# Performance work log

Measured on AMD Instinct MI355X. Metric: run time of the kernel, lower is better.

## Reference

```python
import jax, jax.numpy as jnp
import numpy as np

B = 32; NPG = 500; N = B * NPG; E = 256000; F = 1024; OD = 128
DD = 80; TD = 32; NH = 4; DH = TD // NH; DFF = 128; NL = 2
LSUB = 128; MAXLEN = 4 * LSUB
NEG = -1e9; SLOPE = 0.01; EPS = 1e-5


def setup_inputs() -> dict:
    key = jax.random.key(0)
    ks = iter(jax.random.split(key, 64))
    nrm = lambda *s: jax.random.normal(next(ks), s, jnp.float32)
    w = lambda *s: nrm(*s) * 0.02
    inp = {}
    inp["pro1_x"] = nrm(N, F)
    inp["pro2_x"] = nrm(N, F)
    inp["pro1_edge_index"] = jax.random.randint(next(ks), (2, E), 0, N)
    inp["pro2_edge_index"] = jax.random.randint(next(ks), (2, E), 0, N)
    inp["pro1_batch"] = jnp.repeat(jnp.arange(B), NPG)
    inp["pro2_batch"] = jnp.repeat(jnp.arange(B), NPG)
    for nm in ("mas1_straight", "mas1_flipped", "mas2_straight", "mas2_flipped"):
        inp[nm] = nrm(B, LSUB, DD)
        inp[nm + "_lengths"] = jax.random.randint(next(ks), (B,), 1, LSUB + 1)
    inp["gcn1_w"] = w(F, F); inp["gcn1_b"] = jnp.zeros(F)
    inp["gcn2_w"] = w(F, F); inp["gcn2_b"] = jnp.zeros(F)
    inp["fc1_w"] = w(OD, F); inp["fc1_b"] = jnp.zeros(OD)
    inp["fc2_w"] = w(OD, F); inp["fc2_b"] = jnp.zeros(OD)
    inp["red_w"] = w(TD - 2, DD); inp["red_b"] = jnp.zeros(TD - 2)
    inp["attn_in_w"] = w(NL, 3 * TD, TD); inp["attn_in_b"] = jnp.zeros((NL, 3 * TD))
    inp["attn_out_w"] = w(NL, TD, TD); inp["attn_out_b"] = jnp.zeros((NL, TD))
    inp["ln1_w"] = jnp.ones((NL, TD)); inp["ln1_b"] = jnp.zeros((NL, TD))
    inp["ln2_w"] = jnp.ones((NL, TD)); inp["ln2_b"] = jnp.zeros((NL, TD))
    inp["ff1_w"] = w(NL, DFF, TD); inp["ff1_b"] = jnp.zeros((NL, DFF))
    inp["ff2_w"] = w(NL, TD, DFF); inp["ff2_b"] = jnp.zeros((NL, TD))
    inp["final_w"] = w(1, 2 * OD + TD); inp["final_b"] = jnp.zeros(1)
    return inp


def _leaky(v):
    return jnp.where(v >= 0, v, SLOPE * v)


def _gcn(x, ei, W, b):
    # GCNConv: x' = D^-1/2 (A + I) D^-1/2 (x @ W^T) + b
    sl = jnp.arange(N, dtype=ei.dtype)
    src = jnp.concatenate([ei[0], sl])
    dst = jnp.concatenate([ei[1], sl])
    deg = jax.ops.segment_sum(jnp.ones(src.shape[0], x.dtype), dst, N)
    dinv = jax.lax.rsqrt(deg)
    norm = (dinv[src] * dinv[dst])[:, None]
    h = x @ W.T
    return jax.ops.segment_sum(h[src] * norm, dst, N) + b


def _gmp(x, batch):
    # global mean pool per graph
    s = jax.ops.segment_sum(x, batch, B)
    c = jax.ops.segment_sum(jnp.ones(x.shape[0], x.dtype), batch, B)
    return s / c[:, None]


def _ln(x, w, b):
    m = x.mean(-1, keepdims=True)
    v = ((x - m) ** 2).mean(-1, keepdims=True)
    return (x - m) * jax.lax.rsqrt(v + EPS) * w + b


def _forward(pro1_x, pro1_edge_index, pro1_batch, pro2_x, pro2_edge_index, pro2_batch,
             mas1_straight, mas1_flipped, mas2_straight, mas2_flipped,
             mas1_straight_lengths, mas1_flipped_lengths, mas2_straight_lengths, mas2_flipped_lengths,
             gcn1_w, gcn1_b, fc1_w, fc1_b, gcn2_w, gcn2_b, fc2_w, fc2_b,
             red_w, red_b, attn_in_w, attn_in_b, attn_out_w, attn_out_b,
             ln1_w, ln1_b, ln2_w, ln2_b, ff1_w, ff1_b, ff2_w, ff2_b,
             final_w, final_b):
    # --- graph branches (dropout = identity at inference) ---
    x1 = _leaky(_gcn(pro1_x, pro1_edge_index, gcn1_w, gcn1_b))
    x1 = _leaky(_gmp(x1, pro1_batch) @ fc1_w.T + fc1_b)           # [B, OD]
    x2 = _leaky(_gcn(pro2_x, pro2_edge_index, gcn2_w, gcn2_b))
    x2 = _leaky(_gmp(x2, pro2_batch) @ fc2_w.T + fc2_b)           # [B, OD]

    # --- vectorized ragged pack: project, append indicators, scatter to offsets ---
    inds = ((1.0, 1.0), (0.0, 1.0), (1.0, 0.0), (0.0, 0.0))      # (straight, first)
    mas = (mas1_straight, mas1_flipped, mas2_straight, mas2_flipped)
    lens = (mas1_straight_lengths, mas1_flipped_lengths, mas2_straight_lengths, mas2_flipped_lengths)
    pos = jnp.arange(LSUB)
    brow = jnp.arange(B)[:, None]
    seq = jnp.zeros((B, MAXLEN, TD), jnp.float32)
    off = jnp.zeros((B,), lens[0].dtype)
    for m, l, (si, fi) in zip(mas, lens, inds):
        proj = m @ red_w.T + red_b                                # [B, LSUB, TD-2]
        ones = jnp.ones((B, LSUB, 1), jnp.float32)
        p = jnp.concatenate([proj, si * ones, fi * ones], -1)    # [B, LSUB, TD]
        valid = pos[None, :] < l[:, None]                        # [B, LSUB]
        idx = jnp.where(valid, off[:, None] + pos[None, :], 0)
        seq = seq.at[brow, idx].add(p * valid[..., None])
        off = off + l
    mask = jnp.arange(MAXLEN)[None, :] < off[:, None]            # [B, MAXLEN] True = valid

    # --- post-norm TransformerEncoder (relu FFN, key padding mask) ---
    x_t = seq
    for li in range(NL):
        qkv = x_t @ attn_in_w[li].T + attn_in_b[li]
        q, k, v = jnp.split(qkv, 3, axis=-1)
        q = q.reshape(B, MAXLEN, NH, DH)
        k = k.reshape(B, MAXLEN, NH, DH)
        v = v.reshape(B, MAXLEN, NH, DH)
        scores = jnp.einsum('bqhd,bkhd->bhqk', q, k) / np.float32(np.sqrt(DH))
        scores = jnp.where(mask[:, None, None, :], scores, NEG)
        attn = jax.nn.softmax(scores, axis=-1)
        o = jnp.einsum('bhqk,bkhd->bqhd', attn, v).reshape(B, MAXLEN, TD)
        o = o @ attn_out_w[li].T + attn_out_b[li]
        x_t = _ln(x_t + o, ln1_w[li], ln1_b[li])
        h = jax.nn.relu(x_t @ ff1_w[li].T + ff1_b[li]) @ ff2_w[li].T + ff2_b[li]
        x_t = _ln(x_t + h, ln2_w[li], ln2_b[li])

    mf = mask[..., None].astype(jnp.float32)
    mas_out = (x_t * mf).sum(1) / mf.sum(1)                      # masked mean [B, TD]

    combined = jnp.concatenate([x1, x2, mas_out], axis=1)        # [B, 2*OD + TD]
    return combined @ final_w.T + final_b                        # [B, 1]


def reference(pro1_x, pro1_edge_index, pro1_batch, pro2_x, pro2_edge_index, pro2_batch,
              mas1_straight, mas1_flipped, mas2_straight, mas2_flipped,
              mas1_straight_lengths, mas1_flipped_lengths, mas2_straight_lengths, mas2_flipped_lengths,
              gcn1_w, gcn1_b, fc1_w, fc1_b, gcn2_w, gcn2_b, fc2_w, fc2_b,
              red_w, red_b, attn_in_w, attn_in_b, attn_out_w, attn_out_b,
              ln1_w, ln1_b, ln2_w, ln2_b, ff1_w, ff1_b, ff2_w, ff2_b,
              final_w, final_b):
    return _forward(pro1_x, pro1_edge_index, pro1_batch, pro2_x, pro2_edge_index, pro2_batch,
                    mas1_straight, mas1_flipped, mas2_straight, mas2_flipped,
                    mas1_straight_lengths, mas1_flipped_lengths, mas2_straight_lengths, mas2_flipped_lengths,
                    gcn1_w, gcn1_b, fc1_w, fc1_b, gcn2_w, gcn2_b, fc2_w, fc2_b,
                    red_w, red_b, attn_in_w, attn_in_b, attn_out_w, attn_out_b,
                    ln1_w, ln1_b, ln2_w, ln2_b, ff1_w, ff1_b, ff2_w, ff2_b,
                    final_w, final_b)
```

## Files before the change

kernel.cpp:

```cpp
#include <hip/hip_runtime.h>
#include <stdint.h>

#define N_NODES 16000
#define B_      32
#define NPG_    500
#define E_      256000
#define F_      1024
#define OD_     128
#define DD_     80
#define TD_     32
#define NH_     4
#define DH_     8
#define DFF_    128
#define LSUB_   128
#define MAXLEN_ 512
#define EPS_    1e-5f
#define SLOPE_  0.01f

typedef __bf16 bf16x8 __attribute__((ext_vector_type(8)));
typedef float  f32x4  __attribute__((ext_vector_type(4)));

__device__ __forceinline__ float leaky(float v) { return v >= 0.f ? v : SLOPE_ * v; }

__device__ __forceinline__ unsigned short f2bf(float f) {
  unsigned u = __float_as_uint(f);
  u += 0x7FFFu + ((u >> 16) & 1u);
  return (unsigned short)(u >> 16);
}
__device__ __forceinline__ float bf2f(unsigned short u) {
  return __uint_as_float((unsigned)u << 16);
}

__device__ __forceinline__ void gld_lds16(const void* g, void* l) {
  __builtin_amdgcn_global_load_lds(
      (const __attribute__((address_space(1))) unsigned int*)g,
      (__attribute__((address_space(3))) unsigned int*)l, 16, 0, 0);
}

__global__ void k_f2bf2(const float* __restrict__ in0, const float* __restrict__ in1,
                        unsigned short* __restrict__ out0, unsigned short* __restrict__ out1,
                        int n4) {
  const float* in = blockIdx.y ? in1 : in0;
  unsigned short* out = blockIdx.y ? out1 : out0;
  int i = blockIdx.x * blockDim.x + threadIdx.x;
  int stride = gridDim.x * blockDim.x;
  for (; i < n4; i += stride) {
    float4 v = ((const float4*)in)[i];
    ushort4 o;
    o.x = f2bf(v.x); o.y = f2bf(v.y); o.z = f2bf(v.z); o.w = f2bf(v.w);
    ((ushort4*)out)[i] = o;
  }
}

__global__ __launch_bounds__(256) void k_gemm_bf16(const unsigned short* __restrict__ A,
                                                   const unsigned short* __restrict__ Bw,
                                                   unsigned short* __restrict__ C) {
  const int K = 1024, N = 1024;
  const size_t g = blockIdx.z;
  A  += g * (size_t)N_NODES * K;
  Bw += g * (size_t)K * N;
  C  += g * (size_t)N_NODES * N;
  __shared__ short As[128 * 32];
  __shared__ short Bs[128 * 32];
  const int t    = threadIdx.x;
  const int lane = t & 63, wave = t >> 6;
  const int wrow = wave >> 1, wcol = wave & 1;
  const int quad = lane >> 4, l15 = lane & 15;
  const int mBase = blockIdx.x * 128;
  const int nBase = blockIdx.y * 128;

  f32x4 acc[4][4];
  f32x4 zero = {0.f, 0.f, 0.f, 0.f};
#pragma unroll
  for (int i = 0; i < 4; ++i)
#pragma unroll
    for (int j = 0; j < 4; ++j) acc[i][j] = zero;

  const int r4 = t >> 2;
  const int c4 = (((t & 3) - ((t >> 3) & 3)) & 3) * 8;
  const int rs = ((quad + (l15 >> 1)) & 3) * 8;

  for (int kt = 0; kt < 32; ++kt) {
    const int k0 = kt * 32;
    gld_lds16(&A[(size_t)(mBase + r4) * K + k0 + c4],       &As[t * 8]);
    gld_lds16(&A[(size_t)(mBase + 64 + r4) * K + k0 + c4],  &As[2048 + t * 8]);
    gld_lds16(&Bw[(size_t)(nBase + r4) * K + k0 + c4],      &Bs[t * 8]);
    gld_lds16(&Bw[(size_t)(nBase + 64 + r4) * K + k0 + c4], &Bs[2048 + t * 8]);
    __syncthreads();

    bf16x8 a[4], b[4];
#pragma unroll
    for (int ti = 0; ti < 4; ++ti)
      a[ti] = *(const bf16x8*)&As[(wrow * 64 + ti * 16 + l15) * 32 + rs];
#pragma unroll
    for (int tj = 0; tj < 4; ++tj)
      b[tj] = *(const bf16x8*)&Bs[(wcol * 64 + tj * 16 + l15) * 32 + rs];
#pragma unroll
    for (int ti = 0; ti < 4; ++ti)
#pragma unroll
      for (int tj = 0; tj < 4; ++tj)
        acc[ti][tj] = __builtin_amdgcn_mfma_f32_16x16x32_bf16(a[ti], b[tj], acc[ti][tj], 0, 0, 0);
    __syncthreads();
  }

#pragma unroll
  for (int ti = 0; ti < 4; ++ti)
#pragma unroll
    for (int tj = 0; tj < 4; ++tj)
#pragma unroll
      for (int r = 0; r < 4; ++r) {
        int grow = mBase + wrow * 64 + ti * 16 + quad * 4 + r;
        int gcol = nBase + wcol * 64 + tj * 16 + l15;
        C[(size_t)grow * N + gcol] = f2bf(acc[ti][tj][r]);
      }
}

__global__ void k_hist(const int* __restrict__ ei0, const int* __restrict__ ei1,
                       int* __restrict__ cnt, int e, int n) {
  const int g = blockIdx.y;
  const int* dst = (g ? ei1 : ei0) + e;
  int i = blockIdx.x * 256 + threadIdx.x;
  if (i < e) atomicAdd(&cnt[g * n + dst[i]], 1);
}

__global__ void k_scan(const int* __restrict__ cnt_all, int* __restrict__ rowstart_all,
                       int* __restrict__ cursor_all, float* __restrict__ dinv_all, int n) {
  const int g = blockIdx.x;
  const int* cnt = cnt_all + g * n;
  int* rowstart = rowstart_all + g * (n + 1);
  int* cursor   = cursor_all + g * n;
  float* dinv   = dinv_all + g * n;
  __shared__ int part[256];
  __shared__ int base[257];
  int t = threadIdx.x;
  int chunk = (n + 255) >> 8;
  int s = 0;
  for (int j = 0; j < chunk; ++j) {
    int idx = t * chunk + j;
    if (idx < n) s += cnt[idx];
  }
  part[t] = s;
  __syncthreads();
  if (t == 0) {
    int a = 0;
    for (int i = 0; i < 256; ++i) { base[i] = a; a += part[i]; }
    base[256] = a;
  }
  __syncthreads();
  int a = base[t];
  for (int j = 0; j < chunk; ++j) {
    int idx = t * chunk + j;
    if (idx < n) {
      int c = cnt[idx];
      rowstart[idx] = a; cursor[idx] = a; a += c;
      dinv[idx] = rsqrtf((float)c + 1.0f);
    }
  }
  if (t == 0) rowstart[n] = base[256];
}

__global__ void k_scatter(const int* __restrict__ ei0, const int* __restrict__ ei1,
                          const float* __restrict__ dinv_all, int* __restrict__ cursor_all,
                          int* __restrict__ csr_all, float* __restrict__ csrw_all,
                          int e, int n) {
  const int g = blockIdx.y;
  const int* ei = g ? ei1 : ei0;
  int i = blockIdx.x * 256 + threadIdx.x;
  if (i < e) {
    int s = ei[i], d = ei[e + i];
    int p = atomicAdd(&cursor_all[g * n + d], 1);
    csr_all[(size_t)g * e + p]  = s;
    csrw_all[(size_t)g * e + p] = dinv_all[g * n + s] * dinv_all[g * n + d];
  }
}

__global__ __launch_bounds__(64) void k_gather(const ushort2* __restrict__ h2,
                                               const float* __restrict__ dinv,
                                               const int* __restrict__ rowstart,
                                               const int* __restrict__ csr,
                                               const float* __restrict__ csrw,
                                               ushort2* __restrict__ agg2) {
  const int sl = blockIdx.x;
  const int i  = blockIdx.y;
  const int t  = threadIdx.x;
  __shared__ int   ssrc[64];
  __shared__ float sw[64];
  const float di = dinv[i];
  const size_t fo = (size_t)sl * 64 + t;
  ushort2 sv = h2[(size_t)i * 512 + fo];
  const float selfw = di * di;
  float ax = bf2f(sv.x) * selfw, ay = bf2f(sv.y) * selfw;
  const int beg = rowstart[i], end = rowstart[i + 1];
  for (int base = beg; base < end; base += 64) {
    int c = end - base; if (c > 64) c = 64;
    __syncthreads();
    if (t < c) { ssrc[t] = csr[base + t]; sw[t] = csrw[base + t]; }
    __syncthreads();
    int j = 0;
    for (; j + 4 <= c; j += 4) {
      ushort2 v0 = h2[(size_t)ssrc[j]     * 512 + fo];
      ushort2 v1 = h2[(size_t)ssrc[j + 1] * 512 + fo];
      ushort2 v2 = h2[(size_t)ssrc[j + 2] * 512 + fo];
      ushort2 v3 = h2[(size_t)ssrc[j + 3] * 512 + fo];
      float w0 = sw[j], w1 = sw[j + 1], w2 = sw[j + 2], w3 = sw[j + 3];
      ax += bf2f(v0.x) * w0 + bf2f(v1.x) * w1 + bf2f(v2.x) * w2 + bf2f(v3.x) * w3;
      ay += bf2f(v0.y) * w0 + bf2f(v1.y) * w1 + bf2f(v2.y) * w2 + bf2f(v3.y) * w3;
    }
    for (; j < c; ++j) {
      ushort2 v0 = h2[(size_t)ssrc[j] * 512 + fo];
      float w0 = sw[j];
      ax += bf2f(v0.x) * w0; ay += bf2f(v0.y) * w0;
    }
  }
  ushort2 o; o.x = f2bf(ax); o.y = f2bf(ay);
  agg2[(size_t)i * 512 + fo] = o;
}

__global__ void k_pool(const unsigned short* __restrict__ agg_all,
                       const float* __restrict__ bias0, const float* __restrict__ bias1,
                       float* __restrict__ pooled_all) {
  int f = blockIdx.x * 256 + threadIdx.x;
  int z = blockIdx.z;
  int g = z >> 5, b = z & 31;
  const unsigned short* agg = agg_all + (size_t)g * N_NODES * F_;
  const float* bias = g ? bias1 : bias0;
  float* pooled = pooled_all + (size_t)g * B_ * F_;
  int r0 = blockIdx.y * 100;
  float bf = bias[f];
  float s = 0.f;
  for (int r = 0; r < 100; ++r)
    s += leaky(bf2f(agg[(size_t)(b * NPG_ + r0 + r) * F_ + f]) + bf);
  atomicAdd(&pooled[b * F_ + f], s);
}

__global__ void k_fc(const float* __restrict__ pooled_all,
                     const float* __restrict__ w0, const float* __restrict__ w1,
                     const float* __restrict__ bias0, const float* __restrict__ bias1,
                     float* __restrict__ out0, float* __restrict__ out1) {
  int b = blockIdx.x, o = threadIdx.x, g = blockIdx.y;
  const float* p  = pooled_all + (size_t)g * B_ * F_ + b * F_;
  const float* wr = (g ? w1 : w0) + o * F_;
  const float* bias = g ? bias1 : bias0;
  float* out = g ? out1 : out0;
  float acc = 0.f;
  for (int f = 0; f < F_; ++f) acc += p[f] * wr[f];
  out[b * OD_ + o] = leaky(acc * (1.f / 500.f) + bias[o]);
}

__global__ void k_pack(const float* __restrict__ m0, const float* __restrict__ m1,
                       const float* __restrict__ m2, const float* __restrict__ m3,
                       const int* __restrict__ l0, const int* __restrict__ l1,
                       const int* __restrict__ l2, const int* __restrict__ l3,
                       const float* __restrict__ rw, const float* __restrict__ rb,
                       float* __restrict__ seq) {
  __shared__ float xs[DD_];
  const int p = blockIdx.x, b = blockIdx.y, k = blockIdx.z;
  const float* mas = (k == 0) ? m0 : (k == 1) ? m1 : (k == 2) ? m2 : m3;
  const int*   lk  = (k == 0) ? l0 : (k == 1) ? l1 : (k == 2) ? l2 : l3;
  const int len = lk[b];
  if (p >= len) return;
  int off = 0;
  if (k > 0) off += l0[b];
  if (k > 1) off += l1[b];
  if (k > 2) off += l2[b];
  const int t = threadIdx.x;
  for (int d = t; d < DD_; d += 64) xs[d] = mas[(size_t)(b * LSUB_ + p) * DD_ + d];
  __syncthreads();
  if (t < TD_) {
    float v;
    if (t < TD_ - 2) {
      float a = rb[t];
      const float* w = &rw[t * DD_];
      for (int d = 0; d < DD_; ++d) a += xs[d] * w[d];
      v = a;
    } else if (t == TD_ - 2) {
      v = (k == 0 || k == 2) ? 1.f : 0.f;
    } else {
      v = (k < 2) ? 1.f : 0.f;
    }
    seq[((size_t)b * MAXLEN_ + off + p) * TD_ + t] = v;
  }
}

__global__ void k_totlen(const int* __restrict__ l0, const int* __restrict__ l1,
                         const int* __restrict__ l2, const int* __restrict__ l3,
                         int* __restrict__ tot) {
  int b = threadIdx.x;
  if (b < B_) tot[b] = l0[b] + l1[b] + l2[b] + l3[b];
}

__global__ void k_qkv(const float* __restrict__ xt, const float* __restrict__ w,
                      const float* __restrict__ bias, const int* __restrict__ tot,
                      float* __restrict__ qkv) {
  __shared__ float xs[TD_];
  const int row = blockIdx.x;
  if ((row & (MAXLEN_ - 1)) >= tot[row >> 9]) return;
  const int t = threadIdx.x;
  if (t < TD_) xs[t] = xt[(size_t)row * TD_ + t];
  __syncthreads();
  if (t < 3 * TD_) {
    float a = bias[t];
    const float* wr = &w[t * TD_];
#pragma unroll
    for (int k = 0; k < TD_; ++k) a += xs[k] * wr[k];
    qkv[(size_t)row * 96 + t] = a;
  }
}

__global__ __launch_bounds__(128) void k_attn(const float* __restrict__ qkv,
                                              const int* __restrict__ tot,
                                              float* __restrict__ obuf) {
  __shared__ float Kl[MAXLEN_ * DH_];
  __shared__ float Vl[MAXLEN_ * DH_];
  const int h = blockIdx.x, b = blockIdx.y, qz = blockIdx.z;
  const int t = threadIdx.x;
  const int L = tot[b];
  if (qz * 64 >= L) return;
  const float* base = &qkv[(size_t)b * MAXLEN_ * 96];
  for (int i = t; i < L * DH_; i += 128) {
    int p = i >> 3, d = i & 7;
    Kl[i] = base[p * 96 + 32 + h * 8 + d];
    Vl[i] = base[p * 96 + 64 + h * 8 + d];
  }
  __syncthreads();
  const int qi = qz * 64 + (t >> 1);
  if (qi >= L) return;
  const int half = t & 1;
  const float scale = 0.35355339059327373f;
  float q[8];
#pragma unroll
  for (int d = 0; d < 8; ++d) q[d] = base[qi * 96 + h * 8 + d] * scale;

  float l0 = 0.f, l1 = 0.f;
  float a0[8] = {0, 0, 0, 0, 0, 0, 0, 0};
  float a1[8] = {0, 0, 0, 0, 0, 0, 0, 0};
  int j = half;
  for (; j + 2 < L; j += 4) {
    const float* kr0 = &Kl[j * 8];
    const float* kr1 = &Kl[(j + 2) * 8];
    float s0 = 0.f, s1 = 0.f;
#pragma unroll
    for (int d = 0; d < 8; ++d) { s0 += q[d] * kr0[d]; s1 += q[d] * kr1[d]; }
    float p0 = __expf(s0), p1 = __expf(s1);
    l0 += p0; l1 += p1;
    const float* vr0 = &Vl[j * 8];
    const float* vr1 = &Vl[(j + 2) * 8];
#pragma unroll
    for (int d = 0; d < 8; ++d) { a0[d] += p0 * vr0[d]; a1[d] += p1 * vr1[d]; }
  }
  for (; j < L; j += 2) {
    const float* kr = &Kl[j * 8];
    float s = 0.f;
#pragma unroll
    for (int d = 0; d < 8; ++d) s += q[d] * kr[d];
    float p = __expf(s);
    l0 += p;
    const float* vr = &Vl[j * 8];
#pragma unroll
    for (int d = 0; d < 8; ++d) a0[d] += p * vr[d];
  }
  float l = l0 + l1;
#pragma unroll
  for (int d = 0; d < 8; ++d) a0[d] += a1[d];
  l += __shfl_xor(l, 1);
#pragma unroll
  for (int d = 0; d < 8; ++d) a0[d] += __shfl_xor(a0[d], 1);
  float inv = 1.f / l;
  const int dbase = half * 4;
  float4 o;
  o.x = a0[dbase + 0] * inv; o.y = a0[dbase + 1] * inv;
  o.z = a0[dbase + 2] * inv; o.w = a0[dbase + 3] * inv;
  *(float4*)&obuf[((size_t)b * MAXLEN_ + qi) * TD_ + h * 8 + dbase] = o;
}

__global__ void k_oproj_ln(const float* __restrict__ obuf, const float* __restrict__ w,
                           const float* __restrict__ bias, const float* __restrict__ lw,
                           const float* __restrict__ lb, const int* __restrict__ tot,
                           float* __restrict__ xt) {
  const int t = threadIdx.x;
  const int r = blockIdx.x * 8 + (t >> 5);
  if ((r & (MAXLEN_ - 1)) >= tot[r >> 9]) return;
  const int j = t & 31;
  const float* orow = &obuf[(size_t)r * TD_];
  float a = bias[j] + xt[(size_t)r * TD_ + j];
  const float* wr = &w[j * TD_];
#pragma unroll
  for (int k = 0; k < TD_; ++k) a += orow[k] * wr[k];
  float s1 = a, s2 = a * a;
#pragma unroll
  for (int m = 1; m < 32; m <<= 1) {
    s1 += __shfl_xor(s1, m, 32);
    s2 += __shfl_xor(s2, m, 32);
  }
  float mean = s1 * (1.f / 32.f);
  float var  = s2 * (1.f / 32.f) - mean * mean;
  xt[(size_t)r * TD_ + j] = (a - mean) * rsqrtf(var + EPS_) * lw[j] + lb[j];
}

__global__ void k_ffn_ln(const float* __restrict__ w1, const float* __restrict__ b1,
                         const float* __restrict__ w2, const float* __restrict__ b2,
                         const float* __restrict__ lw, const float* __restrict__ lb,
                         const int* __restrict__ tot, float* __restrict__ xt) {
  const int r = blockIdx.x, t = threadIdx.x;
  if ((r & (MAXLEN_ - 1)) >= tot[r >> 9]) return;
  __shared__ float xs[TD_];
  __shared__ float hb[DFF_];
  if (t < TD_) xs[t] = xt[(size_t)r * TD_ + t];
  __syncthreads();
  {
    float a = b1[t];
    const float* wr = &w1[t * TD_];
#pragma unroll
    for (int k = 0; k < TD_; ++k) a += xs[k] * wr[k];
    hb[t] = fmaxf(a, 0.f);
  }
  __syncthreads();
  if (t < TD_) {
    float a = b2[t] + xs[t];
    const float* wr = &w2[t * DFF_];
#pragma unroll
    for (int k = 0; k < DFF_; ++k) a += hb[k] * wr[k];
    float s1 = a, s2 = a * a;
#pragma unroll
    for (int m = 1; m < 32; m <<= 1) {
      s1 += __shfl_xor(s1, m, 32);
      s2 += __shfl_xor(s2, m, 32);
    }
    float mean = s1 * (1.f / 32.f);
    float var  = s2 * (1.f / 32.f) - mean * mean;
    xt[(size_t)r * TD_ + t] = (a - mean) * rsqrtf(var + EPS_) * lw[t] + lb[t];
  }
}

__global__ void k_maskmean(const float* __restrict__ xt, const int* __restrict__ tot,
                           float* __restrict__ mout) {
  __shared__ float sbuf[8][32];
  const int b = blockIdx.x, t = threadIdx.x;
  const int j = t & 31, c = t >> 5;
  const int L = tot[b];
  float s = 0.f;
  for (int p = c; p < L; p += 8) s += xt[((size_t)b * MAXLEN_ + p) * TD_ + j];
  sbuf[c][j] = s;
  __syncthreads();
  if (t < 32) {
    float a = 0.f;
#pragma unroll
    for (int cc = 0; cc < 8; ++cc) a += sbuf[cc][t];
    mout[b * TD_ + t] = a / (float)L;
  }
}

__global__ void k_final(const float* __restrict__ x1, const float* __restrict__ x2,
                        const float* __restrict__ mo, const float* __restrict__ fw,
                        const float* __restrict__ fb, float* __restrict__ out) {
  const int b = blockIdx.x, t = threadIdx.x;
  float s = 0.f;
  for (int i = t; i < 2 * OD_ + TD_; i += 64) {
    float c = (i < OD_) ? x1[b * OD_ + i]
            : (i < 2 * OD_) ? x2[b * OD_ + (i - OD_)]
            : mo[b * TD_ + (i - 2 * OD_)];
    s += fw[i] * c;
  }
#pragma unroll
  for (int m = 1; m < 64; m <<= 1) s += __shfl_xor(s, m, 64);
  if (t == 0) out[b] = s + fb[0];
}

extern "C" void kernel_launch(void* const* d_in, const int* in_sizes, int n_in,
                              void* d_out, int out_size, void* d_ws, size_t ws_size,
                              hipStream_t stream) {
  (void)in_sizes; (void)n_in; (void)out_size; (void)ws_size;
  const float* pro_x[2]  = {(const float*)d_in[0], (const float*)d_in[1]};
  const int*   pro_ei[2] = {(const int*)d_in[2], (const int*)d_in[3]};
  const float* mas[4]    = {(const float*)d_in[6], (const float*)d_in[8],
                            (const float*)d_in[10], (const float*)d_in[12]};
  const int*   lens[4]   = {(const int*)d_in[7], (const int*)d_in[9],
                            (const int*)d_in[11], (const int*)d_in[13]};
  const float* gw[2]  = {(const float*)d_in[14], (const float*)d_in[16]};
  const float* gb[2]  = {(const float*)d_in[15], (const float*)d_in[17]};
  const float* fcw[2] = {(const float*)d_in[18], (const float*)d_in[20]};
  const float* fcb[2] = {(const float*)d_in[19], (const float*)d_in[21]};
  const float* red_w = (const float*)d_in[22];
  const float* red_b = (const float*)d_in[23];
  const float* attn_in_w  = (const float*)d_in[24];
  const float* attn_in_b  = (const float*)d_in[25];
  const float* attn_out_w = (const float*)d_in[26];
  const float* attn_out_b = (const float*)d_in[27];
  const float* ln1_w = (const float*)d_in[28];
  const float* ln1_b = (const float*)d_in[29];
  const float* ln2_w = (const float*)d_in[30];
  const float* ln2_b = (const float*)d_in[31];
  const float* ff1_w = (const float*)d_in[32];
  const float* ff1_b = (const float*)d_in[33];
  const float* ff2_w = (const float*)d_in[34];
  const float* ff2_b = (const float*)d_in[35];
  const float* final_w = (const float*)d_in[36];
  const float* final_b = (const float*)d_in[37];
  float* out = (float*)d_out;

  char* p = (char*)d_ws;
  auto carve = [&](size_t bytes) -> void* {
    void* r = (void*)p;
    p += (bytes + 255) & ~(size_t)255;
    return r;
  };
  unsigned short* xb  = (unsigned short*)carve((size_t)2 * N_NODES * F_ * 2);
  unsigned short* Wb  = (unsigned short*)carve((size_t)2 * F_ * F_ * 2);
  unsigned short* h   = (unsigned short*)carve((size_t)2 * N_NODES * F_ * 2);
  unsigned short* agg = (unsigned short*)carve((size_t)2 * N_NODES * F_ * 2);
  int*   cnt      = (int*)carve((size_t)2 * N_NODES * 4);
  float* dinv     = (float*)carve((size_t)2 * N_NODES * 4);
  int*   rowstart = (int*)carve((size_t)2 * (N_NODES + 1) * 4);
  int*   cursor   = (int*)carve((size_t)2 * N_NODES * 4);
  int*   csr      = (int*)carve((size_t)2 * E_ * 4);
  float* csrw     = (float*)carve((size_t)2 * E_ * 4);
  float* pooled   = (float*)carve((size_t)2 * B_ * F_ * 4);
  float* xg[2];
  xg[0] = (float*)carve((size_t)B_ * OD_ * 4);
  xg[1] = (float*)carve((size_t)B_ * OD_ * 4);
  float* seq    = (float*)carve((size_t)B_ * MAXLEN_ * TD_ * 4);
  float* qkv    = (float*)carve((size_t)B_ * MAXLEN_ * 96 * 4);
  float* obuf   = (float*)carve((size_t)B_ * MAXLEN_ * TD_ * 4);
  int*   totlen = (int*)carve((size_t)B_ * 4);
  float* masout = (float*)carve((size_t)B_ * TD_ * 4);

  k_f2bf2<<<dim3(1024, 2), 256, 0, stream>>>(pro_x[0], pro_x[1], xb,
                                             xb + (size_t)N_NODES * F_, (N_NODES * F_) / 4);
  k_f2bf2<<<dim3(512, 2), 256, 0, stream>>>(gw[0], gw[1], Wb, Wb + (size_t)F_ * F_,
                                            (F_ * F_) / 4);
  k_gemm_bf16<<<dim3(125, 8, 2), 256, 0, stream>>>(xb, Wb, h);
  hipMemsetAsync(cnt, 0, (size_t)2 * N_NODES * 4, stream);
  k_hist<<<dim3(1000, 2), 256, 0, stream>>>(pro_ei[0], pro_ei[1], cnt, E_, N_NODES);
  k_scan<<<2, 256, 0, stream>>>(cnt, rowstart, cursor, dinv, N_NODES);
  k_scatter<<<dim3(1000, 2), 256, 0, stream>>>(pro_ei[0], pro_ei[1], dinv, cursor,
                                               csr, csrw, E_, N_NODES);
  for (int g = 0; g < 2; ++g) {
    k_gather<<<dim3(8, N_NODES), 64, 0, stream>>>(
        (const ushort2*)(h + (size_t)g * N_NODES * F_), dinv + (size_t)g * N_NODES,
        rowstart + (size_t)g * (N_NODES + 1), csr + (size_t)g * E_, csrw + (size_t)g * E_,
        (ushort2*)(agg + (size_t)g * N_NODES * F_));
  }
  hipMemsetAsync(pooled, 0, (size_t)2 * B_ * F_ * 4, stream);
  k_pool<<<dim3(4, 5, 64), 256, 0, stream>>>(agg, gb[0], gb[1], pooled);
  k_fc<<<dim3(B_, 2), 128, 0, stream>>>(pooled, fcw[0], fcw[1], fcb[0], fcb[1],
                                        xg[0], xg[1]);

  hipMemsetAsync(seq, 0, (size_t)B_ * MAXLEN_ * TD_ * 4, stream);
  k_pack<<<dim3(LSUB_, B_, 4), 64, 0, stream>>>(mas[0], mas[1], mas[2], mas[3],
                                                lens[0], lens[1], lens[2], lens[3],
                                                red_w, red_b, seq);
  k_totlen<<<1, 64, 0, stream>>>(lens[0], lens[1], lens[2], lens[3], totlen);

  for (int li = 0; li < 2; ++li) {
    k_qkv<<<B_ * MAXLEN_, 128, 0, stream>>>(seq, attn_in_w + (size_t)li * 96 * TD_,
                                            attn_in_b + (size_t)li * 96, totlen, qkv);
    k_attn<<<dim3(NH_, B_, 8), 128, 0, stream>>>(qkv, totlen, obuf);
    k_oproj_ln<<<(B_ * MAXLEN_) / 8, 256, 0, stream>>>(
        obuf, attn_out_w + (size_t)li * TD_ * TD_, attn_out_b + (size_t)li * TD_,
        ln1_w + (size_t)li * TD_, ln1_b + (size_t)li * TD_, totlen, seq);
    k_ffn_ln<<<B_ * MAXLEN_, 128, 0, stream>>>(
        ff1_w + (size_t)li * DFF_ * TD_, ff1_b + (size_t)li * DFF_,
        ff2_w + (size_t)li * TD_ * DFF_, ff2_b + (size_t)li * TD_,
        ln2_w + (size_t)li * TD_, ln2_b + (size_t)li * TD_, totlen, seq);
  }

  k_maskmean<<<B_, 256, 0, stream>>>(seq, totlen, masout);
  k_final<<<B_, 64, 0, stream>>>(xg[0], xg[1], masout, final_w, final_b, out);
}
```

Before: 812.9 us.

## Replace 128x128 GEMM with double-buffered 256x256 tile pipelined kernel

Replaces the bf16 GCN feature GEMM with a 512-thread kernel using 256x256 output tiles, a 64-wide K step, and double-buffered LDS filled by direct global-to-LDS loads that overlap with MFMA quadrants under explicit waitcnt and barrier scheduling plus s_setprio. The M dimension is padded to 16128 rows so 256-row tiles divide evenly. The block index is remapped into chunked tile positions for better L2 locality. This aims to raise arithmetic intensity and hide load latency in the dominant GEMM. The cost is heavier register and LDS use and padded rows that are computed but never used.

```diff
diff --git a/kernel.cpp b/kernel.cpp
--- a/kernel.cpp
+++ b/kernel.cpp
@@ -2,6 +2,7 @@
 #include <stdint.h>
 
 #define N_NODES 16000
+#define MPAD_   16128
 #define B_      32
 #define NPG_    500
 #define E_      256000
@@ -52,66 +53,137 @@
   }
 }
 
-__global__ __launch_bounds__(256) void k_gemm_bf16(const unsigned short* __restrict__ A,
-                                                   const unsigned short* __restrict__ Bw,
-                                                   unsigned short* __restrict__ C) {
-  const int K = 1024, N = 1024;
+#define LDSA(bf, ks, row) (*(const bf16x8*)&lds[(bf)*16384 + (ks)*8192 + (row)*32 + rs])
+#define LDSB(bf, ks, row) (*(const bf16x8*)&lds[32768 + (bf)*16384 + (ks)*8192 + (row)*32 + rs])
+#define STG_A(bf, R, kti) do { \
+  gld_lds16(&Ag[(size_t)(mBase + (R) + r4) * 1024 + (kti) * 64 + c4],      &lds[(bf)*16384 + (R)*32 + t*8]); \
+  gld_lds16(&Ag[(size_t)(mBase + (R) + r4) * 1024 + (kti) * 64 + 32 + c4], &lds[(bf)*16384 + 8192 + (R)*32 + t*8]); \
+} while (0)
+#define STG_B(bf, R, kti) do { \
+  gld_lds16(&Bg[(size_t)(nBase + (R) + r4) * 1024 + (kti) * 64 + c4],      &lds[32768 + (bf)*16384 + (R)*32 + t*8]); \
+  gld_lds16(&Bg[(size_t)(nBase + (R) + r4) * 1024 + (kti) * 64 + 32 + c4], &lds[32768 + (bf)*16384 + 8192 + (R)*32 + t*8]); \
+} while (0)
+#define RD_Q0(bf) do { \
+  _Pragma("unroll") for (int mi = 0; mi < 4; ++mi) \
+  _Pragma("unroll") for (int ks = 0; ks < 2; ++ks) \
+    aLo[mi][ks] = LDSA(bf, ks, wrow * 128 + mi * 16 + l15); \
+  _Pragma("unroll") for (int ni = 0; ni < 2; ++ni) \
+  _Pragma("unroll") for (int ks = 0; ks < 2; ++ks) \
+    bLo[ni][ks] = LDSB(bf, ks, wcol * 64 + ni * 16 + l15); \
+} while (0)
+#define RD_BHI(bf) do { \
+  _Pragma("unroll") for (int ni = 0; ni < 2; ++ni) \
+  _Pragma("unroll") for (int ks = 0; ks < 2; ++ks) \
+    bHi[ni][ks] = LDSB(bf, ks, wcol * 64 + (2 + ni) * 16 + l15); \
+} while (0)
+#define RD_AHI(bf) do { \
+  _Pragma("unroll") for (int mi = 0; mi < 4; ++mi) \
+  _Pragma("unroll") for (int ks = 0; ks < 2; ++ks) \
+    aHi[mi][ks] = LDSA(bf, ks, wrow * 128 + (4 + mi) * 16 + l15); \
+} while (0)
+#define MM_Q0() do { __builtin_amdgcn_s_setprio(1); \
+  _Pragma("unroll") for (int mi = 0; mi < 4; ++mi) \
+  _Pragma("unroll") for (int ni = 0; ni < 2; ++ni) \
+  _Pragma("unroll") for (int ks = 0; ks < 2; ++ks) \
+    acc[mi][ni] = __builtin_amdgcn_mfma_f32_16x16x32_bf16(aLo[mi][ks], bLo[ni][ks], acc[mi][ni], 0, 0, 0); \
+  __builtin_amdgcn_s_setprio(0); } while (0)
+#define MM_Q1() do { __builtin_amdgcn_s_setprio(1); \
+  _Pragma("unroll") for (int mi = 0; mi < 4; ++mi) \
+  _Pragma("unroll") for (int ni = 0; ni < 2; ++ni) \
+  _Pragma("unroll") for (int ks = 0; ks < 2; ++ks) \
+    acc[mi][2 + ni] = __builtin_amdgcn_mfma_f32_16x16x32_bf16(aLo[mi][ks], bHi[ni][ks], acc[mi][2 + ni], 0, 0, 0); \
+  __builtin_amdgcn_s_setprio(0); } while (0)
+#define MM_Q3() do { __builtin_amdgcn_s_setprio(1); \
+  _Pragma("unroll") for (int mi = 0; mi < 4; ++mi) \
+  _Pragma("unroll") for (int ni = 0; ni < 2; ++ni) \
+  _Pragma("unroll") for (int ks = 0; ks < 2; ++ks) \
+    acc[4 + mi][2 + ni] = __builtin_amdgcn_mfma_f32_16x16x32_bf16(aHi[mi][ks], bHi[ni][ks], acc[4 + mi][2 + ni], 0, 0, 0); \
+  __builtin_amdgcn_s_setprio(0); } while (0)
+#define MM_Q2() do { __builtin_amdgcn_s_setprio(1); \
+  _Pragma("unroll") for (int mi = 0; mi < 4; ++mi) \
+  _Pragma("unroll") for (int ni = 0; ni < 2; ++ni) \
+  _Pragma("unroll") for (int ks = 0; ks < 2; ++ks) \
+    acc[4 + mi][ni] = __builtin_amdgcn_mfma_f32_16x16x32_bf16(aHi[mi][ks], bLo[ni][ks], acc[4 + mi][ni], 0, 0, 0); \
+  __builtin_amdgcn_s_setprio(0); } while (0)
+#define BAR() do { __builtin_amdgcn_sched_barrier(0); __builtin_amdgcn_s_barrier(); \
+                   __builtin_amdgcn_sched_barrier(0); } while (0)
+#define LGKM0() do { asm volatile("s_waitcnt lgkmcnt(0)" ::: "memory"); \
+                     __builtin_amdgcn_sched_barrier(0); } while (0)
+#define VM4() do { asm volatile("s_waitcnt vmcnt(4)" ::: "memory"); } while (0)
+#define VM0() do { asm volatile("s_waitcnt vmcnt(0)" ::: "memory"); } while (0)
+
+__global__ __launch_bounds__(512, 2) void k_gemm256(const unsigned short* __restrict__ Ag,
+                                                    const unsigned short* __restrict__ Bg,
+                                                    unsigned short* __restrict__ Cg) {
+  __shared__ short lds[65536];
+  const int j  = blockIdx.x;
+  const int x8 = j & 7;
+  const int chunk = (x8 < 4) ? x8 * 32 : 128 + (x8 - 4) * 31;
+  const int pos = chunk + (j >> 3);
+  const int mb = pos >> 2, nb = pos & 3;
   const size_t g = blockIdx.z;
-  A  += g * (size_t)N_NODES * K;
-  Bw += g * (size_t)K * N;
-  C  += g * (size_t)N_NODES * N;
-  __shared__ short As[128 * 32];
-  __shared__ short Bs[128 * 32];
-  const int t    = threadIdx.x;
+  Ag += g * (size_t)MPAD_ * 1024;
+  Bg += g * (size_t)1024 * 1024;
+  Cg += g * (size_t)MPAD_ * 1024;
+  const int t = threadIdx.x;
   const int lane = t & 63, wave = t >> 6;
-  const int wrow = wave >> 1, wcol = wave & 1;
+  const int wrow = wave >> 2, wcol = wave & 3;
   const int quad = lane >> 4, l15 = lane & 15;
-  const int mBase = blockIdx.x * 128;
-  const int nBase = blockIdx.y * 128;
-
-  f32x4 acc[4][4];
-  f32x4 zero = {0.f, 0.f, 0.f, 0.f};
-#pragma unroll
-  for (int i = 0; i < 4; ++i)
-#pragma unroll
-    for (int j = 0; j < 4; ++j) acc[i][j] = zero;
-
+  const int mBase = mb * 256, nBase = nb * 256;
   const int r4 = t >> 2;
   const int c4 = (((t & 3) - ((t >> 3) & 3)) & 3) * 8;
   const int rs = ((quad + (l15 >> 1)) & 3) * 8;
 
-  for (int kt = 0; kt < 32; ++kt) {
-    const int k0 = kt * 32;
-    gld_lds16(&A[(size_t)(mBase + r4) * K + k0 + c4],       &As[t * 8]);
-    gld_lds16(&A[(size_t)(mBase + 64 + r4) * K + k0 + c4],  &As[2048 + t * 8]);
-    gld_lds16(&Bw[(size_t)(nBase + r4) * K + k0 + c4],      &Bs[t * 8]);
-    gld_lds16(&Bw[(size_t)(nBase + 64 + r4) * K + k0 + c4], &Bs[2048 + t * 8]);
-    __syncthreads();
-
-    bf16x8 a[4], b[4];
-#pragma unroll
-    for (int ti = 0; ti < 4; ++ti)
-      a[ti] = *(const bf16x8*)&As[(wrow * 64 + ti * 16 + l15) * 32 + rs];
-#pragma unroll
-    for (int tj = 0; tj < 4; ++tj)
-      b[tj] = *(const bf16x8*)&Bs[(wcol * 64 + tj * 16 + l15) * 32 + rs];
-#pragma unroll
-    for (int ti = 0; ti < 4; ++ti)
-#pragma unroll
-      for (int tj = 0; tj < 4; ++tj)
-        acc[ti][tj] = __builtin_amdgcn_mfma_f32_16x16x32_bf16(a[ti], b[tj], acc[ti][tj], 0, 0, 0);
-    __syncthreads();
-  }
-
-#pragma unroll
-  for (int ti = 0; ti < 4; ++ti)
-#pragma unroll
-    for (int tj = 0; tj < 4; ++tj)
+  f32x4 acc[8][4];
+  f32x4 zero = {0.f, 0.f, 0.f, 0.f};
+#pragma unroll
+  for (int i = 0; i < 8; ++i)
+#pragma unroll
+    for (int jn = 0; jn < 4; ++jn) acc[i][jn] = zero;
+
+  bf16x8 aLo[4][2], aHi[4][2], bLo[2][2], bHi[2][2];
+
+  STG_A(0, 0, 0); STG_A(0, 128, 0); STG_B(0, 0, 0); STG_B(0, 128, 0);
+  STG_B(1, 0, 1); STG_B(1, 128, 1);
+  VM4();
+  BAR();
+
+  for (int kt = 0; kt < 16; kt += 2) {
+    const bool s2 = (kt + 2) < 16;
+    const bool s3 = (kt + 3) < 16;
+    RD_Q0(0);
+    STG_A(1, 0, kt + 1);
+    BAR(); LGKM0(); MM_Q0(); BAR();
+    RD_BHI(0);
+    STG_A(1, 128, kt + 1);
+    BAR(); LGKM0(); MM_Q1(); BAR();
+    RD_AHI(0);
+    if (s2) STG_B(0, 0, kt + 2);
+    BAR(); LGKM0(); MM_Q3(); BAR();
+    if (s2) { STG_B(0, 128, kt + 2); VM4(); } else VM0();
+    BAR(); MM_Q2(); BAR();
+    RD_Q0(1);
+    if (s2) STG_A(0, 0, kt + 2);
+    BAR(); LGKM0(); MM_Q0(); BAR();
+    RD_BHI(1);
+    if (s2) STG_A(0, 128, kt + 2);
+    BAR(); LGKM0(); MM_Q1(); BAR();
+    RD_AHI(1);
+    if (s3) STG_B(1, 0, kt + 3);
+    BAR(); LGKM0(); MM_Q3(); BAR();
+    if (s3) { STG_B(1, 128, kt + 3); VM4(); }
+    BAR(); MM_Q2(); BAR();
+  }
+
+#pragma unroll
+  for (int mi = 0; mi < 8; ++mi)
+#pragma unroll
+    for (int ni = 0; ni < 4; ++ni)
 #pragma unroll
       for (int r = 0; r < 4; ++r) {
-        int grow = mBase + wrow * 64 + ti * 16 + quad * 4 + r;
-        int gcol = nBase + wcol * 64 + tj * 16 + l15;
-        C[(size_t)grow * N + gcol] = f2bf(acc[ti][tj][r]);
+        int grow = mBase + wrow * 128 + mi * 16 + quad * 4 + r;
+        int gcol = nBase + wcol * 64 + ni * 16 + l15;
+        Cg[(size_t)grow * 1024 + gcol] = f2bf(acc[mi][ni][r]);
       }
 }
 
@@ -504,9 +576,9 @@
     p += (bytes + 255) & ~(size_t)255;
     return r;
   };
-  unsigned short* xb  = (unsigned short*)carve((size_t)2 * N_NODES * F_ * 2);
+  unsigned short* xb  = (unsigned short*)carve((size_t)2 * MPAD_ * F_ * 2);
   unsigned short* Wb  = (unsigned short*)carve((size_t)2 * F_ * F_ * 2);
-  unsigned short* h   = (unsigned short*)carve((size_t)2 * N_NODES * F_ * 2);
+  unsigned short* h   = (unsigned short*)carve((size_t)2 * MPAD_ * F_ * 2);
   unsigned short* agg = (unsigned short*)carve((size_t)2 * N_NODES * F_ * 2);
   int*   cnt      = (int*)carve((size_t)2 * N_NODES * 4);
   float* dinv     = (float*)carve((size_t)2 * N_NODES * 4);
@@ -525,10 +597,10 @@
   float* masout = (float*)carve((size_t)B_ * TD_ * 4);
 
   k_f2bf2<<<dim3(1024, 2), 256, 0, stream>>>(pro_x[0], pro_x[1], xb,
-                                             xb + (size_t)N_NODES * F_, (N_NODES * F_) / 4);
+                                             xb + (size_t)MPAD_ * F_, (N_NODES * F_) / 4);
   k_f2bf2<<<dim3(512, 2), 256, 0, stream>>>(gw[0], gw[1], Wb, Wb + (size_t)F_ * F_,
                                             (F_ * F_) / 4);
-  k_gemm_bf16<<<dim3(125, 8, 2), 256, 0, stream>>>(xb, Wb, h);
+  k_gemm256<<<dim3(252, 1, 2), 512, 0, stream>>>(xb, Wb, h);
   hipMemsetAsync(cnt, 0, (size_t)2 * N_NODES * 4, stream);
   k_hist<<<dim3(1000, 2), 256, 0, stream>>>(pro_ei[0], pro_ei[1], cnt, E_, N_NODES);
   k_scan<<<2, 256, 0, stream>>>(cnt, rowstart, cursor, dinv, N_NODES);
@@ -536,7 +608,7 @@
                                                csr, csrw, E_, N_NODES);
   for (int g = 0; g < 2; ++g) {
     k_gather<<<dim3(8, N_NODES), 64, 0, stream>>>(
-        (const ushort2*)(h + (size_t)g * N_NODES * F_), dinv + (size_t)g * N_NODES,
+        (const ushort2*)(h + (size_t)g * MPAD_ * F_), dinv + (size_t)g * N_NODES,
         rowstart + (size_t)g * (N_NODES + 1), csr + (size_t)g * E_, csrw + (size_t)g * E_,
         (ushort2*)(agg + (size_t)g * N_NODES * F_));
   }
```

Measured after the change: 782.9 us. 1.04x faster.
